# Performance work log

Hardware: AMD Instinct MI355X
Metric: run time of the kernel (lower is better)

## Reference

```python
import jax, jax.numpy as jnp
import numpy as np

N_ATOMS = 4096
N_ANGLES = 200000


def setup_inputs() -> dict:
    key = jax.random.key(0)
    k1, k2, k3, k4, k5 = jax.random.split(key, 5)
    # pairwise unit direction vectors [N, N, 3]
    vec = jax.random.normal(k1, (N_ATOMS, N_ATOMS, 3), dtype=jnp.float32)
    vec = vec / jnp.linalg.norm(vec, axis=-1, keepdims=True)
    # pairwise distances [N, N], strictly positive
    dist = jax.random.uniform(k2, (N_ATOMS, N_ATOMS), dtype=jnp.float32) * 2.0 + 0.5
    # angle triplets [A, 3]
    coord_idx = jax.random.randint(k3, (N_ANGLES, 3), 0, N_ATOMS)
    # per-angle parameters: k0 (force const) and theta0 (equilibrium angle, rad)
    k0 = jax.random.uniform(k4, (N_ANGLES,), dtype=jnp.float32) * 100.0
    theta0 = jax.random.uniform(k5, (N_ANGLES,), dtype=jnp.float32) * np.float32(np.pi)
    params = jnp.stack([k0, theta0], axis=1)
    forces_out = jnp.zeros((N_ATOMS, 3), dtype=jnp.float32)
    return {
        "dist_mat": dist,
        "vector_mat": vec,
        "forces_out": forces_out,
        "params": params,
        "coord_idx": coord_idx,
        "calc_energy": 1,
        "calc_forces": 1,
    }


def reference(dist_mat, vector_mat, forces_out, params, coord_idx, calc_energy, calc_forces):
    k0 = params[:, 0]
    theta0 = params[:, 1]
    a1 = coord_idx[:, 0]
    a2 = coord_idx[:, 1]
    a3 = coord_idx[:, 2]

    vec21 = vector_mat[a2, a1]            # [A, 3]
    vec23 = vector_mat[a2, a3]            # [A, 3]
    dist21 = dist_mat[a2, a1]             # [A]
    dist23 = dist_mat[a2, a3]             # [A]

    cos_theta = jnp.clip(jnp.sum(vec21 * vec23, axis=1), -1.0, 1.0)
    theta = jnp.arccos(cos_theta)
    delta_theta = theta - theta0

    if calc_energy:
        energy = jnp.sum(k0 * delta_theta * delta_theta)
    else:
        energy = jnp.zeros([1], dtype=forces_out.dtype)

    forces = forces_out
    if calc_forces:
        sin_theta = jnp.sqrt(1.0 - cos_theta * cos_theta)
        # matches torch nan_to_num(nan=0.0): zero out coef where sin_theta == 0
        coef = jnp.where(sin_theta > 0.0,
                         -2.0 * k0 * delta_theta / jnp.maximum(sin_theta, 1e-12),
                         0.0)
        force0 = coef[:, None] * (cos_theta[:, None] * vec21 - vec23) / dist21[:, None]
        force2 = coef[:, None] * (cos_theta[:, None] * vec23 - vec21) / dist23[:, None]
        force1 = -(force0 + force2)
        forces = forces.at[a1].add(force0).at[a2].add(force1).at[a3].add(force2)

    return energy, forces
```

## Files before the change

kernel.cpp:

```cpp
#include <hip/hip_runtime.h>


__global__ void __launch_bounds__(1024)
angle_kernel(const float*  __restrict__ dist,
             const float*  __restrict__ vec,
             const float2* __restrict__ params,
             const int*    __restrict__ cidx,
             const int*    __restrict__ ce_p,
             const int*    __restrict__ cf_p,
             float* __restrict__ ws_f,
             float* __restrict__ ws_e,
             float* __restrict__ out,
             int n_atoms, int n_angles) {
    extern __shared__ float s_f[];
    __shared__ float s_e;
    const int nf  = n_atoms * 3;
    const int tid = threadIdx.x;

    for (int j = tid; j < nf; j += 1024) s_f[j] = 0.0f;
    if (tid == 0) s_e = 0.0f;
    __syncthreads();

    const int ce = ce_p[0];
    const int cf = cf_p[0];

    float e_acc = 0.0f;
    const int i = blockIdx.x * 1024 + tid;
    if (i < n_angles) {
        const int a1 = cidx[3 * i + 0];
        const int a2 = cidx[3 * i + 1];
        const int a3 = cidx[3 * i + 2];
        const float2 kt = params[i];

        const unsigned row = (unsigned)a2 * (unsigned)n_atoms;
        const unsigned b21 = row + (unsigned)a1;
        const unsigned b23 = row + (unsigned)a3;
        const float* __restrict__ p21 = vec + 3u * b21;
        const float* __restrict__ p23 = vec + 3u * b23;

        const float v21x = p21[0], v21y = p21[1], v21z = p21[2];
        const float v23x = p23[0], v23y = p23[1], v23z = p23[2];
        const float d21 = dist[b21];
        const float d23 = dist[b23];

        float c = v21x * v23x + v21y * v23y + v21z * v23z;
        c = fminf(1.0f, fmaxf(-1.0f, c));
        const float th  = acosf(c);
        const float dth = th - kt.y;

        if (ce) e_acc = kt.x * dth * dth;

        if (cf) {
            const float s2 = fmaxf(0.0f, 1.0f - c * c);
            const float s  = sqrtf(s2);
            const float coef = (s > 0.0f) ? (-2.0f * kt.x * dth / fmaxf(s, 1e-12f)) : 0.0f;
            const float i21 = coef / d21;
            const float i23 = coef / d23;

            const float f0x = i21 * (c * v21x - v23x);
            const float f0y = i21 * (c * v21y - v23y);
            const float f0z = i21 * (c * v21z - v23z);
            const float f2x = i23 * (c * v23x - v21x);
            const float f2y = i23 * (c * v23y - v21y);
            const float f2z = i23 * (c * v23z - v21z);
            const float f1x = -(f0x + f2x);
            const float f1y = -(f0y + f2y);
            const float f1z = -(f0z + f2z);

            atomicAdd(&s_f[a1 * 3 + 0], f0x);
            atomicAdd(&s_f[a1 * 3 + 1], f0y);
            atomicAdd(&s_f[a1 * 3 + 2], f0z);
            atomicAdd(&s_f[a2 * 3 + 0], f1x);
            atomicAdd(&s_f[a2 * 3 + 1], f1y);
            atomicAdd(&s_f[a2 * 3 + 2], f1z);
            atomicAdd(&s_f[a3 * 3 + 0], f2x);
            atomicAdd(&s_f[a3 * 3 + 1], f2y);
            atomicAdd(&s_f[a3 * 3 + 2], f2z);
        }
    }

    for (int off = 32; off > 0; off >>= 1)
        e_acc += __shfl_down(e_acc, off, 64);
    if ((tid & 63) == 0) atomicAdd(&s_e, e_acc);
    __syncthreads();

    if (ws_f != nullptr) {
        float* __restrict__ w = ws_f + (size_t)blockIdx.x * nf;
        for (int j = tid; j < nf; j += 1024) w[j] = s_f[j];
        if (tid == 0) ws_e[blockIdx.x] = s_e;
    } else {
        for (int j = tid; j < nf; j += 1024) {
            const float v = s_f[j];
            if (v != 0.0f) atomicAdd(&out[1 + j], v);
        }
        if (tid == 0) atomicAdd(&out[0], s_e);
    }
}

__global__ void __launch_bounds__(64)
reduce_kernel(const float* __restrict__ ws_f,
              const float* __restrict__ ws_e,
              const float* __restrict__ forces0,
              float* __restrict__ out,
              int nf, int n_part) {
    const int j = blockIdx.x * 64 + threadIdx.x;
    if (j < nf) {
        float s = forces0[j];
        for (int p = 0; p < n_part; ++p)
            s += ws_f[(size_t)p * nf + j];
        out[1 + j] = s;
    }
    if (blockIdx.x == 0) {
        float e = 0.0f;
        for (int p = (int)threadIdx.x; p < n_part; p += 64)
            e += ws_e[p];
        for (int off = 32; off > 0; off >>= 1)
            e += __shfl_down(e, off, 64);
        if (threadIdx.x == 0) out[0] = e;
    }
}

__global__ void init_out_kernel(float* __restrict__ out,
                                const float* __restrict__ forces0,
                                int nf) {
    int j = blockIdx.x * blockDim.x + threadIdx.x;
    if (j == 0) out[0] = 0.0f;
    if (j < nf) out[1 + j] = forces0[j];
}

extern "C" void kernel_launch(void* const* d_in, const int* in_sizes, int n_in,
                              void* d_out, int out_size, void* d_ws, size_t ws_size,
                              hipStream_t stream) {
    const float*  dist    = (const float*)d_in[0];
    const float*  vec     = (const float*)d_in[1];
    const float*  forces0 = (const float*)d_in[2];
    const float2* params  = (const float2*)d_in[3];
    const int*    cidx    = (const int*)d_in[4];
    const int*    ce_p    = (const int*)d_in[5];
    const int*    cf_p    = (const int*)d_in[6];
    float* out = (float*)d_out;

    const int n_atoms  = in_sizes[2] / 3;
    const int n_angles = in_sizes[4] / 3;
    const int nf = n_atoms * 3;

    const int n_part = (n_angles + 1023) / 1024;
    const size_t ws_need = ((size_t)n_part * nf + n_part) * sizeof(float);
    const bool use_ws = (ws_size >= ws_need);

    float* ws_f = use_ws ? (float*)d_ws : nullptr;
    float* ws_e = use_ws ? ((float*)d_ws + (size_t)n_part * nf) : nullptr;

    const size_t lds_bytes = (size_t)nf * sizeof(float);

    if (!use_ws)
        init_out_kernel<<<(nf + 1 + 255) / 256, 256, 0, stream>>>(out, forces0, nf);

    angle_kernel<<<n_part, 1024, lds_bytes, stream>>>(dist, vec, params, cidx,
                                                      ce_p, cf_p, ws_f, ws_e, out,
                                                      n_atoms, n_angles);

    if (use_ws)
        reduce_kernel<<<(nf + 63) / 64, 64, 0, stream>>>(ws_f, ws_e, forces0,
                                                         out, nf, n_part);
}
```

Baseline: 338.0 us.

## Fuse per-block partial reduction into global atomics with staggered flush offsets

```diff
diff --git a/kernel.cpp b/kernel.cpp
--- a/kernel.cpp
+++ b/kernel.cpp
@@ -1,32 +1,45 @@
 #include <hip/hip_runtime.h>
 
 
-__global__ void __launch_bounds__(1024)
-angle_kernel(const float*  __restrict__ dist,
-             const float*  __restrict__ vec,
-             const float2* __restrict__ params,
-             const int*    __restrict__ cidx,
-             const int*    __restrict__ ce_p,
-             const int*    __restrict__ cf_p,
-             float* __restrict__ ws_f,
-             float* __restrict__ ws_e,
-             float* __restrict__ out,
-             int n_atoms, int n_angles) {
+__global__ void init_out_kernel(float* __restrict__ out,
+                                const float* __restrict__ forces0,
+                                int nf) {
+    int j = blockIdx.x * blockDim.x + threadIdx.x;
+    if (j == 0) out[0] = 0.0f;
+    if (j < nf) out[1 + j] = forces0[j];
+}
+
+#define NB 256
+#define NT 1024
+
+__global__ void __launch_bounds__(NT)
+angle_fused_kernel(const float*  __restrict__ dist,
+                   const float*  __restrict__ vec,
+                   const float2* __restrict__ params,
+                   const int*    __restrict__ cidx,
+                   const int*    __restrict__ ce_p,
+                   const int*    __restrict__ cf_p,
+                   float* __restrict__ out,
+                   int n_atoms, int n_angles) {
     extern __shared__ float s_f[];
     __shared__ float s_e;
     const int nf  = n_atoms * 3;
     const int tid = threadIdx.x;
+    const int b   = blockIdx.x;
 
-    for (int j = tid; j < nf; j += 1024) s_f[j] = 0.0f;
+    for (int j = tid; j < nf; j += NT) s_f[j] = 0.0f;
     if (tid == 0) s_e = 0.0f;
     __syncthreads();
 
     const int ce = ce_p[0];
     const int cf = cf_p[0];
 
+    const int i0 = (int)(((long)b * n_angles) / NB);
+    const int i1 = (int)(((long)(b + 1) * n_angles) / NB);
+    const int i  = i0 + tid;
+
     float e_acc = 0.0f;
-    const int i = blockIdx.x * 1024 + tid;
-    if (i < n_angles) {
+    if (i < i1) {
         const int a1 = cidx[3 * i + 0];
         const int a2 = cidx[3 * i + 1];
         const int a3 = cidx[3 * i + 2];
@@ -63,16 +76,13 @@
             const float f2x = i23 * (c * v23x - v21x);
             const float f2y = i23 * (c * v23y - v21y);
             const float f2z = i23 * (c * v23z - v21z);
-            const float f1x = -(f0x + f2x);
-            const float f1y = -(f0y + f2y);
-            const float f1z = -(f0z + f2z);
 
             atomicAdd(&s_f[a1 * 3 + 0], f0x);
             atomicAdd(&s_f[a1 * 3 + 1], f0y);
             atomicAdd(&s_f[a1 * 3 + 2], f0z);
-            atomicAdd(&s_f[a2 * 3 + 0], f1x);
-            atomicAdd(&s_f[a2 * 3 + 1], f1y);
-            atomicAdd(&s_f[a2 * 3 + 2], f1z);
+            atomicAdd(&s_f[a2 * 3 + 0], -(f0x + f2x));
+            atomicAdd(&s_f[a2 * 3 + 1], -(f0y + f2y));
+            atomicAdd(&s_f[a2 * 3 + 2], -(f0z + f2z));
             atomicAdd(&s_f[a3 * 3 + 0], f2x);
             atomicAdd(&s_f[a3 * 3 + 1], f2y);
             atomicAdd(&s_f[a3 * 3 + 2], f2z);
@@ -84,48 +94,17 @@
     if ((tid & 63) == 0) atomicAdd(&s_e, e_acc);
     __syncthreads();
 
-    if (ws_f != nullptr) {
-        float* __restrict__ w = ws_f + (size_t)blockIdx.x * nf;
-        for (int j = tid; j < nf; j += 1024) w[j] = s_f[j];
-        if (tid == 0) ws_e[blockIdx.x] = s_e;
-    } else {
-        for (int j = tid; j < nf; j += 1024) {
+    if (ce && tid == 0) atomicAdd(&out[0], s_e);
+
+    if (cf) {
+        const int base = (b * (nf / NB)) % nf;
+        for (int jj = tid; jj < nf; jj += NT) {
+            int j = jj + base;
+            if (j >= nf) j -= nf;
             const float v = s_f[j];
             if (v != 0.0f) atomicAdd(&out[1 + j], v);
         }
-        if (tid == 0) atomicAdd(&out[0], s_e);
     }
-}
-
-__global__ void __launch_bounds__(64)
-reduce_kernel(const float* __restrict__ ws_f,
-              const float* __restrict__ ws_e,
-              const float* __restrict__ forces0,
-              float* __restrict__ out,
-              int nf, int n_part) {
-    const int j = blockIdx.x * 64 + threadIdx.x;
-    if (j < nf) {
-        float s = forces0[j];
-        for (int p = 0; p < n_part; ++p)
-            s += ws_f[(size_t)p * nf + j];
-        out[1 + j] = s;
-    }
-    if (blockIdx.x == 0) {
-        float e = 0.0f;
-        for (int p = (int)threadIdx.x; p < n_part; p += 64)
-            e += ws_e[p];
-        for (int off = 32; off > 0; off >>= 1)
-            e += __shfl_down(e, off, 64);
-        if (threadIdx.x == 0) out[0] = e;
-    }
-}
-
-__global__ void init_out_kernel(float* __restrict__ out,
-                                const float* __restrict__ forces0,
-                                int nf) {
-    int j = blockIdx.x * blockDim.x + threadIdx.x;
-    if (j == 0) out[0] = 0.0f;
-    if (j < nf) out[1 + j] = forces0[j];
 }
 
 extern "C" void kernel_launch(void* const* d_in, const int* in_sizes, int n_in,
@@ -144,23 +123,10 @@
     const int n_angles = in_sizes[4] / 3;
     const int nf = n_atoms * 3;
 
-    const int n_part = (n_angles + 1023) / 1024;
-    const size_t ws_need = ((size_t)n_part * nf + n_part) * sizeof(float);
-    const bool use_ws = (ws_size >= ws_need);
-
-    float* ws_f = use_ws ? (float*)d_ws : nullptr;
-    float* ws_e = use_ws ? ((float*)d_ws + (size_t)n_part * nf) : nullptr;
+    init_out_kernel<<<(nf + 1 + 255) / 256, 256, 0, stream>>>(out, forces0, nf);
 
     const size_t lds_bytes = (size_t)nf * sizeof(float);
-
-    if (!use_ws)
-        init_out_kernel<<<(nf + 1 + 255) / 256, 256, 0, stream>>>(out, forces0, nf);
-
-    angle_kernel<<<n_part, 1024, lds_bytes, stream>>>(dist, vec, params, cidx,
-                                                      ce_p, cf_p, ws_f, ws_e, out,
+    angle_fused_kernel<<<NB, NT, lds_bytes, stream>>>(dist, vec, params, cidx,
+                                                      ce_p, cf_p, out,
                                                       n_atoms, n_angles);
-
-    if (use_ws)
-        reduce_kernel<<<(nf + 63) / 64, 64, 0, stream>>>(ws_f, ws_e, forces0,
-                                                         out, nf, n_part);
 }
```

Result: faster. 301.0 us (-11.0%).
